# Performance work log

Measured on AMD Instinct MI355X. Metric: run time of the kernel, lower is better.

The kernel has to match this reference:

```python
import jax, jax.numpy as jnp
import numpy as np

N = 50000
E = 500000
IN_DIM = 384
HID = 128
HEADS = 4
OUT_DIM = 384
NEG_SLOPE = 0.2


def gat_conv(x, edge_index, W, att_src, att_dst, bias):
    """PyG GATConv (concat=True, add_self_loops=True, eval mode).
    x: [N, F_in]; edge_index: [2, E] (row 0 = source j, row 1 = target i);
    W: [F_in, H*C]; att_src/att_dst: [H, C]; bias: [H*C].
    """
    n = x.shape[0]
    # add self loops
    loops = jnp.arange(n, dtype=edge_index.dtype)
    src = jnp.concatenate([edge_index[0], loops])
    dst = jnp.concatenate([edge_index[1], loops])

    h = (x @ W).reshape(n, HEADS, -1)              # [N, H, C]
    a_src = jnp.einsum('nhc,hc->nh', h, att_src)   # [N, H]
    a_dst = jnp.einsum('nhc,hc->nh', h, att_dst)   # [N, H]

    e = a_src[src] + a_dst[dst]                    # [E', H]
    e = jax.nn.leaky_relu(e, NEG_SLOPE)
    # segment softmax over incoming edges of each target node
    e_max = jax.ops.segment_max(e, dst, num_segments=n)
    e_exp = jnp.exp(e - e_max[dst])
    denom = jax.ops.segment_sum(e_exp, dst, num_segments=n)
    alpha = e_exp / denom[dst]                     # [E', H]

    msg = h[src] * alpha[:, :, None]               # [E', H, C]
    out = jax.ops.segment_sum(msg, dst, num_segments=n)  # [N, H, C]
    return out.reshape(n, -1) + bias


def setup_inputs() -> dict:
    key = jax.random.key(0)
    ks = jax.random.split(key, 12)
    s_in = 1.0 / np.sqrt(IN_DIM)
    s_h = 1.0 / np.sqrt(HEADS * HID)
    return {
        'x': jax.random.normal(ks[0], (N, IN_DIM), dtype=jnp.float32),
        'edge_index': jax.random.randint(ks[1], (2, E), 0, N, dtype=jnp.int32),
        'W1': jax.random.normal(ks[2], (IN_DIM, HEADS * HID), dtype=jnp.float32) * s_in,
        'a1_src': jax.random.normal(ks[3], (HEADS, HID), dtype=jnp.float32) * s_in,
        'a1_dst': jax.random.normal(ks[4], (HEADS, HID), dtype=jnp.float32) * s_in,
        'b1': jnp.zeros((HEADS * HID,), dtype=jnp.float32),
        'W2': jax.random.normal(ks[5], (HEADS * HID, HEADS * HID), dtype=jnp.float32) * s_h,
        'a2_src': jax.random.normal(ks[6], (HEADS, HID), dtype=jnp.float32) * s_h,
        'a2_dst': jax.random.normal(ks[7], (HEADS, HID), dtype=jnp.float32) * s_h,
        'b2': jnp.zeros((HEADS * HID,), dtype=jnp.float32),
        'Wfc': jax.random.normal(ks[8], (HEADS * HID, OUT_DIM), dtype=jnp.float32) * s_h,
        'bfc': jnp.zeros((OUT_DIM,), dtype=jnp.float32),
    }


def reference(x, edge_index, W1, a1_src, a1_dst, b1, W2, a2_src, a2_dst, b2, Wfc, bfc):
    h = jax.nn.relu(gat_conv(x, edge_index, W1, a1_src, a1_dst, b1))
    h = jax.nn.relu(gat_conv(h, edge_index, W2, a2_src, a2_dst, b2))
    return h @ Wfc + bfc  # [N, OUT_DIM]
```

## Files before the change

kernel.cpp:

```cpp
#include <hip/hip_runtime.h>
#include <cfloat>
#include <cstdint>

#define HEADS 4
#define HIDC 128
#define HC 512
#define NEG 0.2f

typedef _Float16 half8 __attribute__((ext_vector_type(8)));
typedef _Float16 half2v __attribute__((ext_vector_type(2)));
typedef float floatx4 __attribute__((ext_vector_type(4)));

__global__ __launch_bounds__(256) void mfma_gemm(
    const _Float16* __restrict__ A,
    const _Float16* __restrict__ Bt,
    _Float16* __restrict__ Ch,
    float* __restrict__ Cf,
    const float* __restrict__ bias,
    const float* __restrict__ atts,
    const float* __restrict__ attd,
    float* __restrict__ a_src,
    float* __restrict__ a_dst,
    int M, int N, int K)
{
    __shared__ __align__(16) _Float16 As[128 * 32];
    __shared__ __align__(16) _Float16 Bs[128 * 32];

    const int tid = threadIdx.x;
    const int w = tid >> 6;
    const int lane = tid & 63;
    const int wr = (w >> 1) * 64;
    const int wc = (w & 1) * 64;

    const int rowBase = blockIdx.y * 128;
    const int colBase = blockIdx.x * 128;

    const int sRow0 = (w * 2 + 0) * 16 + (lane >> 2);
    const int sRow1 = (w * 2 + 1) * 16 + (lane >> 2);
    const int sCol = (lane & 3) * 8;

    const _Float16* gA0 = A + (size_t)(rowBase + sRow0) * K + sCol;
    const _Float16* gA1 = A + (size_t)(rowBase + sRow1) * K + sCol;
    const _Float16* gB0 = Bt + (size_t)(colBase + sRow0) * K + sCol;
    const _Float16* gB1 = Bt + (size_t)(colBase + sRow1) * K + sCol;

    _Float16* lA0 = &As[(w * 2 + 0) * 512];
    _Float16* lA1 = &As[(w * 2 + 1) * 512];
    _Float16* lB0 = &Bs[(w * 2 + 0) * 512];
    _Float16* lB1 = &Bs[(w * 2 + 1) * 512];

    floatx4 acc[4][4];
#pragma unroll
    for (int i = 0; i < 4; i++)
#pragma unroll
        for (int j = 0; j < 4; j++) acc[i][j] = {0.f, 0.f, 0.f, 0.f};

    const int q = lane >> 4;
    const int l16 = lane & 15;

    for (int k0 = 0; k0 < K; k0 += 32) {
        __builtin_amdgcn_global_load_lds(
            (const __attribute__((address_space(1))) unsigned int*)(gA0 + k0),
            (__attribute__((address_space(3))) unsigned int*)lA0, 16, 0, 0);
        __builtin_amdgcn_global_load_lds(
            (const __attribute__((address_space(1))) unsigned int*)(gA1 + k0),
            (__attribute__((address_space(3))) unsigned int*)lA1, 16, 0, 0);
        __builtin_amdgcn_global_load_lds(
            (const __attribute__((address_space(1))) unsigned int*)(gB0 + k0),
            (__attribute__((address_space(3))) unsigned int*)lB0, 16, 0, 0);
        __builtin_amdgcn_global_load_lds(
            (const __attribute__((address_space(1))) unsigned int*)(gB1 + k0),
            (__attribute__((address_space(3))) unsigned int*)lB1, 16, 0, 0);
        __syncthreads();

        half8 af[4], bf[4];
#pragma unroll
        for (int i = 0; i < 4; i++)
            af[i] = *(const half8*)&As[(wr + i * 16 + l16) * 32 + q * 8];
#pragma unroll
        for (int j = 0; j < 4; j++)
            bf[j] = *(const half8*)&Bs[(wc + j * 16 + l16) * 32 + q * 8];
#pragma unroll
        for (int i = 0; i < 4; i++)
#pragma unroll
            for (int j = 0; j < 4; j++)
                acc[i][j] = __builtin_amdgcn_mfma_f32_16x16x32_f16(af[i], bf[j], acc[i][j], 0, 0, 0);
        __syncthreads();
    }

    if (Ch) {
#pragma unroll
        for (int i = 0; i < 4; i++)
#pragma unroll
            for (int j = 0; j < 4; j++) {
                const int col = colBase + wc + j * 16 + l16;
#pragma unroll
                for (int r = 0; r < 4; r++) {
                    const int row = rowBase + wr + i * 16 + q * 4 + r;
                    if (row < M) Ch[(size_t)row * N + col] = (_Float16)acc[i][j][r];
                }
            }
    }
    if (Cf) {
#pragma unroll
        for (int i = 0; i < 4; i++)
#pragma unroll
            for (int j = 0; j < 4; j++) {
                const int col = colBase + wc + j * 16 + l16;
                const float bb = bias ? bias[col] : 0.f;
#pragma unroll
                for (int r = 0; r < 4; r++) {
                    const int row = rowBase + wr + i * 16 + q * 4 + r;
                    if (row < M) Cf[(size_t)row * N + col] = acc[i][j][r] + bb;
                }
            }
    }

    if (atts) {
        float* ps = (float*)As;
        float* pd = ps + 256;
        const int head = blockIdx.x;
        float as[4], ad[4];
#pragma unroll
        for (int j = 0; j < 4; j++) {
            const int cl = wc + j * 16 + l16;
            as[j] = atts[head * HIDC + cl];
            ad[j] = attd[head * HIDC + cl];
        }
#pragma unroll
        for (int i = 0; i < 4; i++) {
#pragma unroll
            for (int r = 0; r < 4; r++) {
                float s_ = acc[i][0][r] * as[0] + acc[i][1][r] * as[1]
                         + acc[i][2][r] * as[2] + acc[i][3][r] * as[3];
                float d_ = acc[i][0][r] * ad[0] + acc[i][1][r] * ad[1]
                         + acc[i][2][r] * ad[2] + acc[i][3][r] * ad[3];
#pragma unroll
                for (int mk = 1; mk <= 8; mk <<= 1) {
                    s_ += __shfl_xor(s_, mk);
                    d_ += __shfl_xor(d_, mk);
                }
                if (l16 == 0) {
                    const int rloc = wr + i * 16 + q * 4 + r;
                    ps[(wc >> 6) * 128 + rloc] = s_;
                    pd[(wc >> 6) * 128 + rloc] = d_;
                }
            }
        }
        __syncthreads();
        if (tid < 128) {
            const int row = rowBase + tid;
            if (row < M) {
                a_src[(size_t)row * 4 + head] = ps[tid] + ps[128 + tid];
                a_dst[(size_t)row * 4 + head] = pd[tid] + pd[128 + tid];
            }
        }
    }
}

__global__ void convert_x_kernel(const float* __restrict__ x, _Float16* __restrict__ o, size_t nquads)
{
    size_t i = (size_t)blockIdx.x * blockDim.x + threadIdx.x;
    if (i < nquads) {
        float4 v = *(const float4*)(x + i * 4);
        _Float16* p = o + i * 4;
        p[0] = (_Float16)v.x; p[1] = (_Float16)v.y;
        p[2] = (_Float16)v.z; p[3] = (_Float16)v.w;
    }
}

__global__ void convert_wT_kernel(const float* __restrict__ W, _Float16* __restrict__ Wt, int K, int N)
{
    int k = blockIdx.x * 64 + (threadIdx.x & 63);
    int n = blockIdx.y * 4 + (threadIdx.x >> 6);
    if (k < K && n < N) Wt[(size_t)n * K + k] = (_Float16)W[(size_t)k * N + n];
}

__global__ void count_kernel(const int* __restrict__ dst, int* __restrict__ deg, int E)
{
    int e = blockIdx.x * blockDim.x + threadIdx.x;
    if (e < E) atomicAdd(&deg[dst[e]], 1);
}

__global__ __launch_bounds__(256) void block_sum_kernel(
    const int* __restrict__ deg, int* __restrict__ bsum, int Nn)
{
    int gid = blockIdx.x * 256 + threadIdx.x;
    int v = (gid < Nn) ? deg[gid] : 0;
#pragma unroll
    for (int o = 32; o >= 1; o >>= 1) v += __shfl_xor(v, o);
    __shared__ int ws[4];
    if ((threadIdx.x & 63) == 0) ws[threadIdx.x >> 6] = v;
    __syncthreads();
    if (threadIdx.x == 0) bsum[blockIdx.x] = ws[0] + ws[1] + ws[2] + ws[3];
}

__global__ __launch_bounds__(256) void scan_bsum_kernel(
    const int* __restrict__ bsum, int* __restrict__ bbase, int nb)
{
    __shared__ int s[256];
    const int tid = threadIdx.x;
    int v = (tid < nb) ? bsum[tid] : 0;
    s[tid] = v;
    __syncthreads();
    for (int off = 1; off < 256; off <<= 1) {
        int t = (tid >= off) ? s[tid - off] : 0;
        __syncthreads();
        s[tid] += t;
        __syncthreads();
    }
    if (tid < nb) bbase[tid] = s[tid] - v;
}

__global__ __launch_bounds__(256) void fill_rowptr_kernel(
    const int* __restrict__ deg, const int* __restrict__ bbase,
    int* __restrict__ rowptr, int* __restrict__ cursor, int Nn, int E)
{
    __shared__ int s[256];
    const int tid = threadIdx.x;
    const int gid = blockIdx.x * 256 + tid;
    int v = (gid < Nn) ? deg[gid] : 0;
    s[tid] = v;
    __syncthreads();
    for (int off = 1; off < 256; off <<= 1) {
        int t = (tid >= off) ? s[tid - off] : 0;
        __syncthreads();
        s[tid] += t;
        __syncthreads();
    }
    if (gid < Nn) {
        int r = bbase[blockIdx.x] + s[tid] - v;
        rowptr[gid] = r;
        cursor[gid] = r;
    }
    if (gid == 0) rowptr[Nn] = E;
}

__global__ void fill_kernel(const int* __restrict__ src, const int* __restrict__ dst,
                            int* __restrict__ cursor, int* __restrict__ eidx,
                            int* __restrict__ edst, int E)
{
    int e = blockIdx.x * blockDim.x + threadIdx.x;
    if (e < E) {
        int d = dst[e];
        int pos = atomicAdd(&cursor[d], 1);
        eidx[pos] = src[e];
        edst[pos] = d;
    }
}

__global__ __launch_bounds__(256) void edge_weight_kernel(
    const int* __restrict__ eidx, const int* __restrict__ edst,
    const float* __restrict__ a_src, const float* __restrict__ a_dst,
    float4* __restrict__ wedge, int E)
{
    int p = blockIdx.x * 256 + threadIdx.x;
    if (p < E) {
        int s = eidx[p];
        int d = edst[p];
        float4 as4 = *(const float4*)(a_src + (size_t)s * 4);
        float4 ad4 = *(const float4*)(a_dst + (size_t)d * 4);
        float l0 = as4.x + ad4.x; l0 = l0 > 0.f ? l0 : NEG * l0;
        float l1 = as4.y + ad4.y; l1 = l1 > 0.f ? l1 : NEG * l1;
        float l2 = as4.z + ad4.z; l2 = l2 > 0.f ? l2 : NEG * l2;
        float l3 = as4.w + ad4.w; l3 = l3 > 0.f ? l3 : NEG * l3;
        wedge[p] = make_float4(__expf(l0), __expf(l1), __expf(l2), __expf(l3));
    }
}

__global__ __launch_bounds__(256) void gather_kernel(
    const _Float16* __restrict__ h, const float* __restrict__ a_src,
    const float* __restrict__ a_dst,
    const int* __restrict__ rowptr, const int* __restrict__ eidx,
    const float4* __restrict__ wedge,
    const float* __restrict__ bias, _Float16* __restrict__ out)
{
    const int node = blockIdx.x;
    const int tid = threadIdx.x;
    const int wv = tid >> 6;
    const int lane = tid & 63;

    __shared__ __align__(16) float4 wgt[256];
    __shared__ int sidx[256];
    __shared__ float accs[4][HC];
    __shared__ float part[4][4];

    const int beg = rowptr[node];
    const int nE = rowptr[node + 1] - beg;
    const int total = nE + 1;

    float acc[8];
#pragma unroll
    for (int i = 0; i < 8; i++) acc[i] = 0.f;
    float4 dsum = make_float4(0.f, 0.f, 0.f, 0.f);

    const int hd = lane >> 4;
    const _Float16* hrow_base = h + (size_t)lane * 8;

    for (int off = 0; off < total; off += 256) {
        const int clen = min(total - off, 256);
        if (tid < clen) {
            const int e = off + tid;
            float4 w4;
            int s;
            if (e == nE) {
                s = node;
                float4 as4 = *(const float4*)(a_src + (size_t)node * 4);
                float4 ad4 = *(const float4*)(a_dst + (size_t)node * 4);
                float l0 = as4.x + ad4.x; l0 = l0 > 0.f ? l0 : NEG * l0;
                float l1 = as4.y + ad4.y; l1 = l1 > 0.f ? l1 : NEG * l1;
                float l2 = as4.z + ad4.z; l2 = l2 > 0.f ? l2 : NEG * l2;
                float l3 = as4.w + ad4.w; l3 = l3 > 0.f ? l3 : NEG * l3;
                w4 = make_float4(__expf(l0), __expf(l1), __expf(l2), __expf(l3));
            } else {
                s = eidx[beg + e];
                w4 = wedge[beg + e];
            }
            sidx[tid] = s;
            wgt[tid] = w4;
            dsum.x += w4.x; dsum.y += w4.y; dsum.z += w4.z; dsum.w += w4.w;
        }
        __syncthreads();
        int e = wv;
        for (; e + 4 < clen; e += 8) {
            const int s0 = sidx[e];
            const int s1 = sidx[e + 4];
            const float w0 = ((const float*)&wgt[e])[hd];
            const float w1 = ((const float*)&wgt[e + 4])[hd];
            half8 hv0 = *(const half8*)(hrow_base + (size_t)s0 * HC);
            half8 hv1 = *(const half8*)(hrow_base + (size_t)s1 * HC);
#pragma unroll
            for (int i = 0; i < 8; i++) acc[i] += w0 * (float)hv0[i];
#pragma unroll
            for (int i = 0; i < 8; i++) acc[i] += w1 * (float)hv1[i];
        }
        if (e < clen) {
            const int s0 = sidx[e];
            const float w0 = ((const float*)&wgt[e])[hd];
            half8 hv0 = *(const half8*)(hrow_base + (size_t)s0 * HC);
#pragma unroll
            for (int i = 0; i < 8; i++) acc[i] += w0 * (float)hv0[i];
        }
        __syncthreads();
    }

#pragma unroll
    for (int o = 32; o >= 1; o >>= 1) {
        dsum.x += __shfl_xor(dsum.x, o);
        dsum.y += __shfl_xor(dsum.y, o);
        dsum.z += __shfl_xor(dsum.z, o);
        dsum.w += __shfl_xor(dsum.w, o);
    }
    if (lane == 0) {
        part[wv][0] = dsum.x; part[wv][1] = dsum.y;
        part[wv][2] = dsum.z; part[wv][3] = dsum.w;
    }
    float* ap = &accs[wv][lane * 8];
#pragma unroll
    for (int i = 0; i < 8; i++) ap[i] = acc[i];
    __syncthreads();

    const int ch = tid * 2;
    const int head = tid >> 6;
    const float is = 1.f / (part[0][head] + part[1][head] + part[2][head] + part[3][head]);
    float t0 = accs[0][ch] + accs[1][ch] + accs[2][ch] + accs[3][ch];
    float t1 = accs[0][ch + 1] + accs[1][ch + 1] + accs[2][ch + 1] + accs[3][ch + 1];
    float2 bv = *(const float2*)(bias + ch);
    float o0 = t0 * is + bv.x; o0 = o0 > 0.f ? o0 : 0.f;
    float o1 = t1 * is + bv.y; o1 = o1 > 0.f ? o1 : 0.f;
    half2v ov; ov.x = (_Float16)o0; ov.y = (_Float16)o1;
    *(half2v*)(out + (size_t)node * HC + ch) = ov;
}

extern "C" void kernel_launch(void* const* d_in, const int* in_sizes, int n_in,
                              void* d_out, int out_size, void* d_ws, size_t ws_size,
                              hipStream_t stream)
{
    const float* x   = (const float*)d_in[0];
    const int*   ei  = (const int*)d_in[1];
    const float* W1  = (const float*)d_in[2];
    const float* a1s = (const float*)d_in[3];
    const float* a1d = (const float*)d_in[4];
    const float* b1  = (const float*)d_in[5];
    const float* W2  = (const float*)d_in[6];
    const float* a2s = (const float*)d_in[7];
    const float* a2d = (const float*)d_in[8];
    const float* b2  = (const float*)d_in[9];
    const float* Wfc = (const float*)d_in[10];
    const float* bfc = (const float*)d_in[11];
    float* out = (float*)d_out;

    const int Nn  = in_sizes[0] / 384;
    const int E   = in_sizes[1] / 2;
    const int IN  = 384;
    const int OUT = in_sizes[11];
    const int Mp  = ((Nn + 127) / 128) * 128;
    const int nb  = (Nn + 255) / 256;

    uint8_t* p = (uint8_t*)d_ws;
    auto alloc = [&](size_t bytes) {
        uint8_t* r = p;
        p += (bytes + 255) & ~(size_t)255;
        return r;
    };
    _Float16* Ah_x = (_Float16*)alloc((size_t)Mp * IN * 2);
    _Float16* Ah_g = (_Float16*)alloc((size_t)Mp * HC * 2);
    _Float16* Hh   = (_Float16*)alloc((size_t)Mp * HC * 2);
    _Float16* Wt1  = (_Float16*)alloc((size_t)HC * IN * 2);
    _Float16* Wt2  = (_Float16*)alloc((size_t)HC * HC * 2);
    _Float16* Wt3  = (_Float16*)alloc((size_t)OUT * HC * 2);
    float* a_src   = (float*)alloc((size_t)Nn * 4 * 4);
    float* a_dst   = (float*)alloc((size_t)Nn * 4 * 4);
    int* deg       = (int*)alloc((size_t)Nn * 4);
    int* rowptr    = (int*)alloc((size_t)(Nn + 1) * 4);
    int* cursor    = (int*)alloc((size_t)Nn * 4);
    int* eidx      = (int*)alloc((size_t)E * 4);
    int* edst      = (int*)alloc((size_t)E * 4);
    float4* wedge  = (float4*)alloc((size_t)E * 16);
    int* bsum      = (int*)alloc((size_t)nb * 4);
    int* bbase     = (int*)alloc((size_t)nb * 4);

    const int* e_src = ei;
    const int* e_dst = ei + E;

    {
        size_t nq = (size_t)Nn * IN / 4;
        convert_x_kernel<<<(nq + 255) / 256, 256, 0, stream>>>(x, Ah_x, nq);
        dim3 gw1((IN + 63) / 64, HC / 4);
        convert_wT_kernel<<<gw1, 256, 0, stream>>>(W1, Wt1, IN, HC);
        dim3 gw2((HC + 63) / 64, HC / 4);
        convert_wT_kernel<<<gw2, 256, 0, stream>>>(W2, Wt2, HC, HC);
        dim3 gw3((HC + 63) / 64, OUT / 4);
        convert_wT_kernel<<<gw3, 256, 0, stream>>>(Wfc, Wt3, HC, OUT);
    }

    hipMemsetAsync(deg, 0, Nn * sizeof(int), stream);
    const int eb = (E + 255) / 256;
    count_kernel<<<eb, 256, 0, stream>>>(e_dst, deg, E);
    block_sum_kernel<<<nb, 256, 0, stream>>>(deg, bsum, Nn);
    scan_bsum_kernel<<<1, 256, 0, stream>>>(bsum, bbase, nb);
    fill_rowptr_kernel<<<nb, 256, 0, stream>>>(deg, bbase, rowptr, cursor, Nn, E);
    fill_kernel<<<eb, 256, 0, stream>>>(e_src, e_dst, cursor, eidx, edst, E);

    const dim3 gg1(HC / 128, Mp / 128);

    mfma_gemm<<<gg1, 256, 0, stream>>>(Ah_x, Wt1, Hh, nullptr, nullptr,
                                       a1s, a1d, a_src, a_dst, Nn, HC, IN);
    edge_weight_kernel<<<eb, 256, 0, stream>>>(eidx, edst, a_src, a_dst, wedge, E);
    gather_kernel<<<Nn, 256, 0, stream>>>(Hh, a_src, a_dst, rowptr, eidx, wedge, b1, Ah_g);

    mfma_gemm<<<gg1, 256, 0, stream>>>(Ah_g, Wt2, Hh, nullptr, nullptr,
                                       a2s, a2d, a_src, a_dst, Nn, HC, HC);
    edge_weight_kernel<<<eb, 256, 0, stream>>>(eidx, edst, a_src, a_dst, wedge, E);
    gather_kernel<<<Nn, 256, 0, stream>>>(Hh, a_src, a_dst, rowptr, eidx, wedge, b2, Ah_g);

    const dim3 gg3(OUT / 128, Mp / 128);
    mfma_gemm<<<gg3, 256, 0, stream>>>(Ah_g, Wt3, nullptr, out, bfc,
                                       nullptr, nullptr, nullptr, nullptr, Nn, OUT, HC);
}
```

Baseline: 595.7 us.

## Fuse edge-weight computation into gather and assign one wavefront per node

Removes the separate edge_weight kernel and the edst/wedge buffers, and instead computes the leaky-ReLU and exp attention weights inline inside the gather from a_src and a_dst. The gather is restructured so that each 64-lane wavefront handles one destination node, four nodes per block. This drops the shared-memory staging, the block syncs and the cross-wave reduction. The cost is that the exp is recomputed per lane group and there is less parallelism per node, with each wave walking its own edge list serially.

```diff
diff --git a/kernel.cpp b/kernel.cpp
--- a/kernel.cpp
+++ b/kernel.cpp
@@ -237,34 +237,13 @@
 }
 
 __global__ void fill_kernel(const int* __restrict__ src, const int* __restrict__ dst,
-                            int* __restrict__ cursor, int* __restrict__ eidx,
-                            int* __restrict__ edst, int E)
+                            int* __restrict__ cursor, int* __restrict__ eidx, int E)
 {
     int e = blockIdx.x * blockDim.x + threadIdx.x;
     if (e < E) {
         int d = dst[e];
         int pos = atomicAdd(&cursor[d], 1);
         eidx[pos] = src[e];
-        edst[pos] = d;
-    }
-}
-
-__global__ __launch_bounds__(256) void edge_weight_kernel(
-    const int* __restrict__ eidx, const int* __restrict__ edst,
-    const float* __restrict__ a_src, const float* __restrict__ a_dst,
-    float4* __restrict__ wedge, int E)
-{
-    int p = blockIdx.x * 256 + threadIdx.x;
-    if (p < E) {
-        int s = eidx[p];
-        int d = edst[p];
-        float4 as4 = *(const float4*)(a_src + (size_t)s * 4);
-        float4 ad4 = *(const float4*)(a_dst + (size_t)d * 4);
-        float l0 = as4.x + ad4.x; l0 = l0 > 0.f ? l0 : NEG * l0;
-        float l1 = as4.y + ad4.y; l1 = l1 > 0.f ? l1 : NEG * l1;
-        float l2 = as4.z + ad4.z; l2 = l2 > 0.f ? l2 : NEG * l2;
-        float l3 = as4.w + ad4.w; l3 = l3 > 0.f ? l3 : NEG * l3;
-        wedge[p] = make_float4(__expf(l0), __expf(l1), __expf(l2), __expf(l3));
     }
 }
 
@@ -272,104 +251,74 @@
     const _Float16* __restrict__ h, const float* __restrict__ a_src,
     const float* __restrict__ a_dst,
     const int* __restrict__ rowptr, const int* __restrict__ eidx,
-    const float4* __restrict__ wedge,
-    const float* __restrict__ bias, _Float16* __restrict__ out)
-{
-    const int node = blockIdx.x;
-    const int tid = threadIdx.x;
-    const int wv = tid >> 6;
-    const int lane = tid & 63;
-
-    __shared__ __align__(16) float4 wgt[256];
-    __shared__ int sidx[256];
-    __shared__ float accs[4][HC];
-    __shared__ float part[4][4];
+    const float* __restrict__ bias, _Float16* __restrict__ out, int Nn)
+{
+    const int wv = __builtin_amdgcn_readfirstlane(threadIdx.x >> 6);
+    const int node = blockIdx.x * 4 + wv;
+    if (node >= Nn) return;
+    const int lane = threadIdx.x & 63;
+    const int hd = lane >> 4;
 
     const int beg = rowptr[node];
-    const int nE = rowptr[node + 1] - beg;
-    const int total = nE + 1;
+    const int deg = rowptr[node + 1] - beg;
+
+    const float ad = a_dst[(size_t)node * 4 + hd];
+    const _Float16* hb = h + (size_t)lane * 8;
 
     float acc[8];
 #pragma unroll
     for (int i = 0; i < 8; i++) acc[i] = 0.f;
-    float4 dsum = make_float4(0.f, 0.f, 0.f, 0.f);
-
-    const int hd = lane >> 4;
-    const _Float16* hrow_base = h + (size_t)lane * 8;
-
-    for (int off = 0; off < total; off += 256) {
-        const int clen = min(total - off, 256);
-        if (tid < clen) {
-            const int e = off + tid;
-            float4 w4;
-            int s;
-            if (e == nE) {
-                s = node;
-                float4 as4 = *(const float4*)(a_src + (size_t)node * 4);
-                float4 ad4 = *(const float4*)(a_dst + (size_t)node * 4);
-                float l0 = as4.x + ad4.x; l0 = l0 > 0.f ? l0 : NEG * l0;
-                float l1 = as4.y + ad4.y; l1 = l1 > 0.f ? l1 : NEG * l1;
-                float l2 = as4.z + ad4.z; l2 = l2 > 0.f ? l2 : NEG * l2;
-                float l3 = as4.w + ad4.w; l3 = l3 > 0.f ? l3 : NEG * l3;
-                w4 = make_float4(__expf(l0), __expf(l1), __expf(l2), __expf(l3));
-            } else {
-                s = eidx[beg + e];
-                w4 = wedge[beg + e];
-            }
-            sidx[tid] = s;
-            wgt[tid] = w4;
-            dsum.x += w4.x; dsum.y += w4.y; dsum.z += w4.z; dsum.w += w4.w;
-        }
-        __syncthreads();
-        int e = wv;
-        for (; e + 4 < clen; e += 8) {
-            const int s0 = sidx[e];
-            const int s1 = sidx[e + 4];
-            const float w0 = ((const float*)&wgt[e])[hd];
-            const float w1 = ((const float*)&wgt[e + 4])[hd];
-            half8 hv0 = *(const half8*)(hrow_base + (size_t)s0 * HC);
-            half8 hv1 = *(const half8*)(hrow_base + (size_t)s1 * HC);
-#pragma unroll
-            for (int i = 0; i < 8; i++) acc[i] += w0 * (float)hv0[i];
-#pragma unroll
-            for (int i = 0; i < 8; i++) acc[i] += w1 * (float)hv1[i];
-        }
-        if (e < clen) {
-            const int s0 = sidx[e];
-            const float w0 = ((const float*)&wgt[e])[hd];
-            half8 hv0 = *(const half8*)(hrow_base + (size_t)s0 * HC);
-#pragma unroll
-            for (int i = 0; i < 8; i++) acc[i] += w0 * (float)hv0[i];
-        }
-        __syncthreads();
-    }
-
-#pragma unroll
-    for (int o = 32; o >= 1; o >>= 1) {
-        dsum.x += __shfl_xor(dsum.x, o);
-        dsum.y += __shfl_xor(dsum.y, o);
-        dsum.z += __shfl_xor(dsum.z, o);
-        dsum.w += __shfl_xor(dsum.w, o);
-    }
-    if (lane == 0) {
-        part[wv][0] = dsum.x; part[wv][1] = dsum.y;
-        part[wv][2] = dsum.z; part[wv][3] = dsum.w;
-    }
-    float* ap = &accs[wv][lane * 8];
-#pragma unroll
-    for (int i = 0; i < 8; i++) ap[i] = acc[i];
-    __syncthreads();
-
-    const int ch = tid * 2;
-    const int head = tid >> 6;
-    const float is = 1.f / (part[0][head] + part[1][head] + part[2][head] + part[3][head]);
-    float t0 = accs[0][ch] + accs[1][ch] + accs[2][ch] + accs[3][ch];
-    float t1 = accs[0][ch + 1] + accs[1][ch + 1] + accs[2][ch + 1] + accs[3][ch + 1];
-    float2 bv = *(const float2*)(bias + ch);
-    float o0 = t0 * is + bv.x; o0 = o0 > 0.f ? o0 : 0.f;
-    float o1 = t1 * is + bv.y; o1 = o1 > 0.f ? o1 : 0.f;
-    half2v ov; ov.x = (_Float16)o0; ov.y = (_Float16)o1;
-    *(half2v*)(out + (size_t)node * HC + ch) = ov;
+    float dsum = 0.f;
+
+    {
+        const float as = a_src[(size_t)node * 4 + hd];
+        half8 hv = *(const half8*)(hb + (size_t)node * HC);
+        float l = as + ad; l = l > 0.f ? l : NEG * l;
+        const float w = __expf(l);
+        dsum += w;
+#pragma unroll
+        for (int i = 0; i < 8; i++) acc[i] += w * (float)hv[i];
+    }
+
+    int e = 0;
+    for (; e + 2 <= deg; e += 2) {
+        const int s0 = eidx[beg + e];
+        const int s1 = eidx[beg + e + 1];
+        half8 hv0 = *(const half8*)(hb + (size_t)s0 * HC);
+        half8 hv1 = *(const half8*)(hb + (size_t)s1 * HC);
+        const float as0 = a_src[(size_t)s0 * 4 + hd];
+        const float as1 = a_src[(size_t)s1 * 4 + hd];
+        float l0 = as0 + ad; l0 = l0 > 0.f ? l0 : NEG * l0;
+        float l1 = as1 + ad; l1 = l1 > 0.f ? l1 : NEG * l1;
+        const float w0 = __expf(l0);
+        const float w1 = __expf(l1);
+        dsum += w0 + w1;
+#pragma unroll
+        for (int i = 0; i < 8; i++) acc[i] += w0 * (float)hv0[i];
+#pragma unroll
+        for (int i = 0; i < 8; i++) acc[i] += w1 * (float)hv1[i];
+    }
+    if (e < deg) {
+        const int s0 = eidx[beg + e];
+        half8 hv0 = *(const half8*)(hb + (size_t)s0 * HC);
+        const float as0 = a_src[(size_t)s0 * 4 + hd];
+        float l0 = as0 + ad; l0 = l0 > 0.f ? l0 : NEG * l0;
+        const float w0 = __expf(l0);
+        dsum += w0;
+#pragma unroll
+        for (int i = 0; i < 8; i++) acc[i] += w0 * (float)hv0[i];
+    }
+
+    const float is = 1.f / dsum;
+    const float* bp = bias + lane * 8;
+    half8 ov;
+#pragma unroll
+    for (int i = 0; i < 8; i++) {
+        float o = acc[i] * is + bp[i];
+        o = o > 0.f ? o : 0.f;
+        ov[i] = (_Float16)o;
+    }
+    *(half8*)(out + (size_t)node * HC + (size_t)lane * 8) = ov;
 }
 
 extern "C" void kernel_launch(void* const* d_in, const int* in_sizes, int n_in,
@@ -415,8 +364,6 @@
     int* rowptr    = (int*)alloc((size_t)(Nn + 1) * 4);
     int* cursor    = (int*)alloc((size_t)Nn * 4);
     int* eidx      = (int*)alloc((size_t)E * 4);
-    int* edst      = (int*)alloc((size_t)E * 4);
-    float4* wedge  = (float4*)alloc((size_t)E * 16);
     int* bsum      = (int*)alloc((size_t)nb * 4);
     int* bbase     = (int*)alloc((size_t)nb * 4);
 
@@ -440,19 +387,18 @@
     block_sum_kernel<<<nb, 256, 0, stream>>>(deg, bsum, Nn);
     scan_bsum_kernel<<<1, 256, 0, stream>>>(bsum, bbase, nb);
     fill_rowptr_kernel<<<nb, 256, 0, stream>>>(deg, bbase, rowptr, cursor, Nn, E);
-    fill_kernel<<<eb, 256, 0, stream>>>(e_src, e_dst, cursor, eidx, edst, E);
+    fill_kernel<<<eb, 256, 0, stream>>>(e_src, e_dst, cursor, eidx, E);
 
     const dim3 gg1(HC / 128, Mp / 128);
+    const int gb = (Nn + 3) / 4;
 
     mfma_gemm<<<gg1, 256, 0, stream>>>(Ah_x, Wt1, Hh, nullptr, nullptr,
                                        a1s, a1d, a_src, a_dst, Nn, HC, IN);
-    edge_weight_kernel<<<eb, 256, 0, stream>>>(eidx, edst, a_src, a_dst, wedge, E);
-    gather_kernel<<<Nn, 256, 0, stream>>>(Hh, a_src, a_dst, rowptr, eidx, wedge, b1, Ah_g);
+    gather_kernel<<<gb, 256, 0, stream>>>(Hh, a_src, a_dst, rowptr, eidx, b1, Ah_g, Nn);
 
     mfma_gemm<<<gg1, 256, 0, stream>>>(Ah_g, Wt2, Hh, nullptr, nullptr,
                                        a2s, a2d, a_src, a_dst, Nn, HC, HC);
-    edge_weight_kernel<<<eb, 256, 0, stream>>>(eidx, edst, a_src, a_dst, wedge, E);
-    gather_kernel<<<Nn, 256, 0, stream>>>(Hh, a_src, a_dst, rowptr, eidx, wedge, b2, Ah_g);
+    gather_kernel<<<gb, 256, 0, stream>>>(Hh, a_src, a_dst, rowptr, eidx, b2, Ah_g, Nn);
 
     const dim3 gg3(OUT / 128, Mp / 128);
     mfma_gemm<<<gg3, 256, 0, stream>>>(Ah_g, Wt3, nullptr, out, bfc,
```

After: 564.5 us. -5.2%, faster.
